# Performance work log

Measured on AMD Instinct MI355X. Metric: run time of the kernel, lower is better.

The kernel has to match this reference:

```python
import jax, jax.numpy as jnp
import numpy as np

B, S, D = 2, 2048, 1024
N_HEADS = 16
HEAD_DIM = D // N_HEADS  # 64, even for RoPE
THETA = 10000.0


def rope_tables(seq, head_dim, dtype=jnp.float32):
    half = head_dim // 2
    freqs = 1.0 / (THETA ** (jnp.arange(half, dtype=jnp.float32) / half))
    angles = jnp.arange(seq, dtype=jnp.float32)[:, None] * freqs[None, :]  # [S, half]
    return jnp.cos(angles).astype(dtype), jnp.sin(angles).astype(dtype)


def apply_rope_interleaved(x, cos, sin):
    # x: [b, h, s, d]; even/odd interleaving
    x_even = x[..., 0::2]
    x_odd = x[..., 1::2]
    r_even = x_even * cos - x_odd * sin
    r_odd = x_even * sin + x_odd * cos
    # interleave back: stack on last axis then reshape
    out = jnp.stack([r_even, r_odd], axis=-1).reshape(x.shape)
    return out


def setup_inputs() -> dict:
    key = jax.random.key(0)
    ks = jax.random.split(key, 6)
    scale = 1.0 / np.sqrt(D)
    return {
        "x": jax.random.normal(ks[0], (B, S, D), dtype=jnp.float32),
        "Wq": jax.random.normal(ks[1], (D, D), dtype=jnp.float32) * scale,
        "Wk": jax.random.normal(ks[2], (D, D), dtype=jnp.float32) * scale,
        "Wv": jax.random.normal(ks[3], (D, D), dtype=jnp.float32) * scale,
        "Wo": jax.random.normal(ks[4], (D, D), dtype=jnp.float32) * scale,
        "bo": jnp.zeros((D,), dtype=jnp.float32),
    }


def reference(x, Wq, Wk, Wv, Wo, bo):
    b, s, _ = x.shape
    # QKV projections (no bias), split heads -> [b, h, s, hd]
    def proj(W):
        return jnp.einsum('bsd,de->bse', x, W).reshape(b, s, N_HEADS, HEAD_DIM).transpose(0, 2, 1, 3)
    q, k, v = proj(Wq), proj(Wk), proj(Wv)

    cos, sin = rope_tables(s, HEAD_DIM, x.dtype)  # [s, hd//2]
    q = apply_rope_interleaved(q, cos, sin)
    k = apply_rope_interleaved(k, cos, sin)

    scale = 1.0 / jnp.sqrt(jnp.asarray(HEAD_DIM, dtype=x.dtype))
    scores = jnp.einsum('bhqd,bhkd->bhqk', q, k) * scale  # [b, h, s, s]
    causal = jnp.tril(jnp.ones((s, s), dtype=bool))
    scores = jnp.where(causal[None, None], scores, jnp.asarray(-jnp.inf, dtype=scores.dtype))
    attn = jax.nn.softmax(scores, axis=-1)
    ctx = jnp.einsum('bhqk,bhkd->bhqd', attn, v)  # [b, h, s, hd]
    ctx = ctx.transpose(0, 2, 1, 3).reshape(b, s, N_HEADS * HEAD_DIM)
    return jnp.einsum('bsd,de->bse', ctx, Wo) + bo
```

## Files before the change

### kernel.cpp

```cpp
#include <hip/hip_runtime.h>
#include <hip/hip_bf16.h>
#include <math.h>

constexpr int Bb   = 2;
constexpr int S    = 2048;
constexpr int D    = 1024;
constexpr int H    = 16;
constexpr int Dh   = 64;
constexpr int HALF = 32;
constexpr int M    = Bb * S;
constexpr int K    = 1024;
constexpr int N    = 1024;

typedef __attribute__((ext_vector_type(8))) short short8;
typedef __attribute__((ext_vector_type(4))) float f32x4;

__device__ __forceinline__ unsigned short f2bf(float f) {
    unsigned int u = __float_as_uint(f);
    unsigned int r = (u + 0x7fffu + ((u >> 16) & 1u)) >> 16;
    return (unsigned short)r;
}

__device__ __forceinline__ void gl_lds16(const unsigned short* g, unsigned short* lds_base) {
    __builtin_amdgcn_global_load_lds(
        (const __attribute__((address_space(1))) unsigned int*)g,
        (__attribute__((address_space(3))) unsigned int*)lds_base, 16, 0, 0);
}

__global__ __launch_bounds__(256) void prep_kernel(
    const float* __restrict__ x,
    const float* W0, const float* W1, const float* W2, const float* W3,
    unsigned short* __restrict__ xb,
    unsigned short* T0, unsigned short* T1, unsigned short* T2, unsigned short* T3,
    float* __restrict__ cosT, float* __restrict__ sinT)
{
    __shared__ float tile[64][65];
    const int bid = blockIdx.x;
    const int tid = threadIdx.x;

    if (bid < 256) {
        int idx = bid * 256 + tid;
        int s = idx >> 5;
        int i = idx & 31;
        double freq = exp(-(double)i * (log(10000.0) / 32.0));
        double ang  = (double)s * freq;
        cosT[idx] = (float)cos(ang);
        sinT[idx] = (float)sin(ang);
    } else if (bid < 256 + 4096) {
        size_t i = (size_t)(bid - 256) * 256 + tid;
        float4 v = *(const float4*)(x + i * 4);
        ushort4 pk;
        pk.x = f2bf(v.x); pk.y = f2bf(v.y); pk.z = f2bf(v.z); pk.w = f2bf(v.w);
        *(ushort4*)(xb + i * 4) = pk;
    } else {
        int wb = bid - 4352;
        int z  = wb >> 8;
        int rem = wb & 255;
        const float* W = (z == 0) ? W0 : (z == 1) ? W1 : (z == 2) ? W2 : W3;
        unsigned short* T = (z == 0) ? T0 : (z == 1) ? T1 : (z == 2) ? T2 : T3;
        const int bk = (rem >> 4) * 64;
        const int bn = (rem & 15) * 64;
        const int lr = tid >> 4;
        const int lc = (tid & 15) * 4;

        #pragma unroll
        for (int i = 0; i < 4; ++i) {
            int r = lr + i * 16;
            float4 v = *(const float4*)(W + (size_t)(bk + r) * N + bn + lc);
            tile[r][lc + 0] = v.x; tile[r][lc + 1] = v.y;
            tile[r][lc + 2] = v.z; tile[r][lc + 3] = v.w;
        }
        __syncthreads();
        #pragma unroll
        for (int i = 0; i < 4; ++i) {
            int nr = lr + i * 16;
            ushort4 pk;
            pk.x = f2bf(tile[lc + 0][nr]);
            pk.y = f2bf(tile[lc + 1][nr]);
            pk.z = f2bf(tile[lc + 2][nr]);
            pk.w = f2bf(tile[lc + 3][nr]);
            *(ushort4*)(T + (size_t)(bn + nr) * K + bk + lc) = pk;
        }
    }
}

__global__ __launch_bounds__(512, 2) void gemm_qkv_kernel(
    const unsigned short* __restrict__ A,
    const unsigned short* __restrict__ BT,
    unsigned short* outQ, unsigned short* outK, unsigned short* outV,
    const float* __restrict__ cosT, const float* __restrict__ sinT)
{
    constexpr int NT    = 16;
    constexpr int ASLOT = 256 * 64;
    constexpr int BSLOT = 192 * 64;
    __shared__ __align__(16) unsigned short As[2 * ASLOT];
    __shared__ __align__(16) unsigned short Bs[2 * BSLOT];

    const int tid  = threadIdx.x;
    const int wid  = tid >> 6;
    const int lane = tid & 63;
    const int col  = lane & 15;
    const int quad = lane >> 4;
    const int wr   = wid >> 2;
    const int wc   = wid & 3;

    const int mbase = blockIdx.y * 256;
    const int nbase = blockIdx.x * 192;

    const int srow8 = lane >> 3;
    const int sch8  = lane & 7;
    const unsigned short *pA[4], *pB[3];
    unsigned short *dA[4], *dB[3];
    #pragma unroll
    for (int w = 0; w < 4; ++w) {
        int r = wid * 32 + w * 8 + srow8;
        pA[w] = A + (size_t)(mbase + r) * K + ((sch8 + (r >> 1)) & 7) * 8;
        dA[w] = &As[(wid * 32 + w * 8) * 64];
    }
    #pragma unroll
    for (int w = 0; w < 3; ++w) {
        int r = wid * 24 + w * 8 + srow8;
        pB[w] = BT + (size_t)(nbase + r) * K + ((sch8 + (r >> 1)) & 7) * 8;
        dB[w] = &Bs[(wid * 24 + w * 8) * 64];
    }

    int aoff[2][8], boff[2][3];
    #pragma unroll
    for (int kh = 0; kh < 2; ++kh) {
        #pragma unroll
        for (int f = 0; f < 8; ++f) {
            int r = wr * 128 + f * 16 + col;
            aoff[kh][f] = r * 64 + (((kh * 4 + quad) - (r >> 1)) & 7) * 8;
        }
        #pragma unroll
        for (int n = 0; n < 3; ++n) {
            int r = wc * 48 + n * 16 + col;
            boff[kh][n] = r * 64 + (((kh * 4 + quad) - (r >> 1)) & 7) * 8;
        }
    }

    f32x4 acc[8][3];
    #pragma unroll
    for (int f = 0; f < 8; ++f)
        #pragma unroll
        for (int n = 0; n < 3; ++n) acc[f][n] = (f32x4)0.f;

    auto stageA = [&](int slot) {
        #pragma unroll
        for (int w = 0; w < 4; ++w) { gl_lds16(pA[w], dA[w] + slot * ASLOT); pA[w] += 64; }
    };
    auto stageB = [&](int slot) {
        #pragma unroll
        for (int w = 0; w < 3; ++w) { gl_lds16(pB[w], dB[w] + slot * BSLOT); pB[w] += 64; }
    };

    stageA(0); stageB(0);
    asm volatile("s_waitcnt vmcnt(0)" ::: "memory");
    __builtin_amdgcn_s_barrier();
    __builtin_amdgcn_sched_barrier(0);

    #pragma unroll 1
    for (int t = 0; t < NT; ++t) {
        const unsigned short* Ab = &As[(t & 1) * ASLOT];
        const unsigned short* Bc = &Bs[(t & 1) * BSLOT];
        const int ns = (t + 1) & 1;
        short8 af[4], bf[3];

        #pragma unroll
        for (int i = 0; i < 4; ++i) af[i] = *(const short8*)&Ab[aoff[0][i]];
        #pragma unroll
        for (int n = 0; n < 3; ++n) bf[n] = *(const short8*)&Bc[boff[0][n]];
        if (t < NT - 1) stageA(ns);
        __builtin_amdgcn_sched_barrier(0);
        __builtin_amdgcn_s_barrier();
        asm volatile("s_waitcnt lgkmcnt(0)" ::: "memory");
        __builtin_amdgcn_s_setprio(1);
        #pragma unroll
        for (int i = 0; i < 4; ++i)
            #pragma unroll
            for (int n = 0; n < 3; ++n)
                acc[i][n] = __builtin_amdgcn_mfma_f32_16x16x32_bf16(af[i], bf[n], acc[i][n], 0, 0, 0);
        __builtin_amdgcn_s_setprio(0);
        __builtin_amdgcn_sched_barrier(0);
        __builtin_amdgcn_s_barrier();
        __builtin_amdgcn_sched_barrier(0);

        #pragma unroll
        for (int i = 0; i < 4; ++i) af[i] = *(const short8*)&Ab[aoff[0][4 + i]];
        if (t < NT - 1) stageB(ns);
        __builtin_amdgcn_sched_barrier(0);
        __builtin_amdgcn_s_barrier();
        asm volatile("s_waitcnt lgkmcnt(0)" ::: "memory");
        __builtin_amdgcn_s_setprio(1);
        #pragma unroll
        for (int i = 0; i < 4; ++i)
            #pragma unroll
            for (int n = 0; n < 3; ++n)
                acc[4 + i][n] = __builtin_amdgcn_mfma_f32_16x16x32_bf16(af[i], bf[n], acc[4 + i][n], 0, 0, 0);
        __builtin_amdgcn_s_setprio(0);
        __builtin_amdgcn_sched_barrier(0);
        __builtin_amdgcn_s_barrier();
        __builtin_amdgcn_sched_barrier(0);

        #pragma unroll
        for (int i = 0; i < 4; ++i) af[i] = *(const short8*)&Ab[aoff[1][i]];
        #pragma unroll
        for (int n = 0; n < 3; ++n) bf[n] = *(const short8*)&Bc[boff[1][n]];
        __builtin_amdgcn_sched_barrier(0);
        __builtin_amdgcn_s_barrier();
        asm volatile("s_waitcnt lgkmcnt(0)" ::: "memory");
        __builtin_amdgcn_s_setprio(1);
        #pragma unroll
        for (int i = 0; i < 4; ++i)
            #pragma unroll
            for (int n = 0; n < 3; ++n)
                acc[i][n] = __builtin_amdgcn_mfma_f32_16x16x32_bf16(af[i], bf[n], acc[i][n], 0, 0, 0);
        __builtin_amdgcn_s_setprio(0);
        __builtin_amdgcn_sched_barrier(0);
        __builtin_amdgcn_s_barrier();
        __builtin_amdgcn_sched_barrier(0);

        #pragma unroll
        for (int i = 0; i < 4; ++i) af[i] = *(const short8*)&Ab[aoff[1][4 + i]];
        __builtin_amdgcn_sched_barrier(0);
        __builtin_amdgcn_s_barrier();
        asm volatile("s_waitcnt lgkmcnt(0)" ::: "memory");
        __builtin_amdgcn_s_setprio(1);
        #pragma unroll
        for (int i = 0; i < 4; ++i)
            #pragma unroll
            for (int n = 0; n < 3; ++n)
                acc[4 + i][n] = __builtin_amdgcn_mfma_f32_16x16x32_bf16(af[i], bf[n], acc[4 + i][n], 0, 0, 0);
        __builtin_amdgcn_s_setprio(0);
        if (t < NT - 1) { asm volatile("s_waitcnt vmcnt(0)" ::: "memory"); }
        __builtin_amdgcn_sched_barrier(0);
        __builtin_amdgcn_s_barrier();
        __builtin_amdgcn_sched_barrier(0);
    }

    #pragma unroll
    for (int n = 0; n < 3; ++n) {
        int n_g = nbase + wc * 48 + n * 16 + col;
        int z   = n_g >> 10;
        int nl  = n_g & 1023;
        int h = nl >> 6, dh0 = nl & 63;
        if (z < 2) {
            unsigned short* o = z ? outK : outQ;
            int p = dh0 >> 1;
            bool even = !(dh0 & 1);
            #pragma unroll
            for (int f = 0; f < 8; ++f)
                #pragma unroll
                for (int reg = 0; reg < 4; ++reg) {
                    int m_g = mbase + wr * 128 + f * 16 + quad * 4 + reg;
                    int b = m_g >> 11, s = m_g & 2047;
                    float v = acc[f][n][reg];
                    float part = __shfl_xor(v, 1, 64);
                    float c = cosT[s * HALF + p], sn = sinT[s * HALF + p];
                    float r = even ? (v * c - part * sn) : (v * c + part * sn);
                    o[((size_t)(b * H + h) * S + s) * Dh + dh0] = f2bf(r);
                }
        } else {
            #pragma unroll
            for (int f = 0; f < 8; ++f) {
                int m0 = mbase + wr * 128 + f * 16 + quad * 4;
                int b = m0 >> 11, s = m0 & 2047;
                ushort4 pk;
                pk.x = f2bf(acc[f][n][0]);
                pk.y = f2bf(acc[f][n][1]);
                pk.z = f2bf(acc[f][n][2]);
                pk.w = f2bf(acc[f][n][3]);
                *(ushort4*)&outV[((size_t)(b * H + h) * Dh + dh0) * S + s] = pk;
            }
        }
    }
}

__global__ __launch_bounds__(256) void gemm_out_kernel(
    const unsigned short* __restrict__ A,
    const unsigned short* __restrict__ BT,
    float* __restrict__ outO, const float* __restrict__ bias)
{
    constexpr int BK   = 64;
    constexpr int ABUF = 64 * BK;
    constexpr int BBUF = 64 * BK;
    __shared__ __align__(16) unsigned short As[2 * ABUF];
    __shared__ __align__(16) unsigned short Bs[2 * BBUF];

    const int tid  = threadIdx.x;
    const int wave = tid >> 6;
    const int lane = tid & 63;
    const int col  = lane & 15;
    const int quad = lane >> 4;
    const int wy   = wave >> 1;
    const int wx   = wave & 1;

    const int mbase = blockIdx.y * 64;
    const int nbase = blockIdx.x * 64;

    const int srow8 = lane >> 3;
    const int sch8  = lane & 7;

    const unsigned short *pA[2], *pB[2];
    unsigned short *dA[2], *dB[2];
    #pragma unroll
    for (int w = 0; w < 2; ++w) {
        int base = wave * 16 + w * 8;
        int tr = base + srow8;
        pA[w] = A  + (size_t)(mbase + tr) * K + ((sch8 + (tr >> 1)) & 7) * 8;
        pB[w] = BT + (size_t)(nbase + tr) * K + ((sch8 + (tr >> 1)) & 7) * 8;
        dA[w] = &As[base * BK];
        dB[w] = &Bs[base * BK];
    }

    int aoff[2][2], boff[2][2];
    #pragma unroll
    for (int ks = 0; ks < 2; ++ks) {
        #pragma unroll
        for (int mi = 0; mi < 2; ++mi) {
            int r = wy * 32 + mi * 16 + col;
            aoff[ks][mi] = r * BK + (((ks * 4 + quad) - (r >> 1)) & 7) * 8;
        }
        #pragma unroll
        for (int ni = 0; ni < 2; ++ni) {
            int r = wx * 32 + ni * 16 + col;
            boff[ks][ni] = r * BK + (((ks * 4 + quad) - (r >> 1)) & 7) * 8;
        }
    }

    f32x4 acc[2][2];
    #pragma unroll
    for (int mi = 0; mi < 2; ++mi)
        #pragma unroll
        for (int ni = 0; ni < 2; ++ni) acc[mi][ni] = (f32x4)0.f;

    auto stage = [&](int buf) {
        #pragma unroll
        for (int w = 0; w < 2; ++w) { gl_lds16(pA[w], dA[w] + buf * ABUF); pA[w] += BK; }
        #pragma unroll
        for (int w = 0; w < 2; ++w) { gl_lds16(pB[w], dB[w] + buf * BBUF); pB[w] += BK; }
    };
    auto compute = [&](int buf) {
        const unsigned short* Ac = &As[buf * ABUF];
        const unsigned short* Bc = &Bs[buf * BBUF];
        #pragma unroll
        for (int ks = 0; ks < 2; ++ks) {
            short8 af[2], bfr[2];
            #pragma unroll
            for (int mi = 0; mi < 2; ++mi) af[mi] = *(const short8*)&Ac[aoff[ks][mi]];
            #pragma unroll
            for (int ni = 0; ni < 2; ++ni) bfr[ni] = *(const short8*)&Bc[boff[ks][ni]];
            #pragma unroll
            for (int mi = 0; mi < 2; ++mi)
                #pragma unroll
                for (int ni = 0; ni < 2; ++ni)
                    acc[mi][ni] = __builtin_amdgcn_mfma_f32_16x16x32_bf16(af[mi], bfr[ni], acc[mi][ni], 0, 0, 0);
        }
    };

    stage(0);
    #pragma unroll 1
    for (int kk = 0; kk < 16; kk += 2) {
        __syncthreads();
        if (kk + 1 < 16) stage(1);
        compute(0);
        __syncthreads();
        if (kk + 2 < 16) stage(0);
        compute(1);
    }

    #pragma unroll
    for (int ni = 0; ni < 2; ++ni) {
        int n_g = nbase + wx * 32 + ni * 16 + col;
        float bv = bias[n_g];
        #pragma unroll
        for (int mi = 0; mi < 2; ++mi)
            #pragma unroll
            for (int reg = 0; reg < 4; ++reg) {
                int m_g = mbase + wy * 32 + mi * 16 + quad * 4 + reg;
                outO[(size_t)m_g * N + n_g] = acc[mi][ni][reg] + bv;
            }
    }
}

__global__ __launch_bounds__(512, 4) void attn_mfma_kernel(
    const unsigned short* __restrict__ q, const unsigned short* __restrict__ k,
    const unsigned short* __restrict__ vt,
    float* __restrict__ Opart, float* __restrict__ lpart)
{
    constexpr int TSZ = 64 * 64;
    __shared__ __align__(16) unsigned short Ks[2 * TSZ];
    __shared__ __align__(16) unsigned short Vs[2 * TSZ];
    __shared__ __align__(16) unsigned short Ps[8][16 * 64];

    const int tid  = threadIdx.x;
    const int wave = tid >> 6;
    const int lane = tid & 63;
    const int col  = lane & 15;
    const int quad = lane >> 4;
    const int r8   = lane >> 3, cp = lane & 7;

    const int pairh = blockIdx.x;
    const int pair  = pairh >> 1;
    const int hpar  = pairh & 1;
    const int bh = blockIdx.y;
    const unsigned short* qb = q  + (size_t)bh * S * Dh;
    const unsigned short* kb = k  + (size_t)bh * S * Dh;
    const unsigned short* vb = vt + (size_t)bh * Dh * S;

    unsigned short* dk = &Ks[(wave * 8) * 64];
    unsigned short* dv = &Vs[(wave * 8) * 64];

    int foff[2][4];
    #pragma unroll
    for (int ks = 0; ks < 2; ++ks)
        #pragma unroll
        for (int nt = 0; nt < 4; ++nt) {
            int r = nt * 16 + col;
            foff[ks][nt] = r * 64 + (((ks * 4 + quad) - r) & 7) * 8;
        }
    int poffW[4][4];
    #pragma unroll
    for (int nt = 0; nt < 4; ++nt)
        #pragma unroll
        for (int reg = 0; reg < 4; ++reg) {
            int row = quad * 4 + reg;
            poffW[nt][reg] = row * 64 + (((nt * 2 + (col >> 3)) ^ (row & 7)) << 3) + (col & 7);
        }
    int poffR[2];
    #pragma unroll
    for (int ks = 0; ks < 2; ++ks)
        poffR[ks] = col * 64 + (((ks * 4 + quad) ^ (col & 7)) << 3);

    for (int phase = 0; phase < 2; ++phase) {
        const int qt  = phase ? (15 - pair) : pair;
        const int wr0 = qt * 128 + wave * 16;
        const int NV  = qt + 1;

        const unsigned short *pk, *pv;
        {
            int r = wave * 8 + r8;
            pk = kb + (size_t)(hpar * 64 + r) * Dh + ((cp + r) & 7) * 8;
            pv = vb + (size_t)r * S + hpar * 64 + ((cp + r) & 7) * 8;
        }
        auto stageKV = [&](int buf) {
            gl_lds16(pk, dk + buf * TSZ);
            gl_lds16(pv, dv + buf * TSZ);
            pk += 128 * Dh;
            pv += 128;
        };

        __syncthreads();
        stageKV(0);

        short8 qfrag[2];
        #pragma unroll
        for (int ks = 0; ks < 2; ++ks)
            qfrag[ks] = *(const short8*)(qb + (size_t)(wr0 + col) * Dh + ks * 32 + quad * 8);

        f32x4 O[4];
        float lacc[4];
        #pragma unroll
        for (int nt = 0; nt < 4; ++nt) O[nt] = (f32x4)0.f;
        #pragma unroll
        for (int r = 0; r < 4; ++r) lacc[r] = 0.f;

        auto subtile = [&](const unsigned short* Kc, const unsigned short* Vc, int t) {
            f32x4 sacc[4];
            #pragma unroll
            for (int nt = 0; nt < 4; ++nt) sacc[nt] = (f32x4)0.f;
            #pragma unroll
            for (int ks = 0; ks < 2; ++ks)
                #pragma unroll
                for (int nt = 0; nt < 4; ++nt) {
                    short8 kf = *(const short8*)&Kc[foff[ks][nt]];
                    sacc[nt] = __builtin_amdgcn_mfma_f32_16x16x32_bf16(qfrag[ks], kf, sacc[nt], 0, 0, 0);
                }
            const bool edge = (t * 64 + 63 > wr0);
            float pb[4][4];
            #pragma unroll
            for (int nt = 0; nt < 4; ++nt) {
                int key_g = t * 64 + nt * 16 + col;
                #pragma unroll
                for (int reg = 0; reg < 4; ++reg) {
                    float e = __builtin_amdgcn_exp2f(
                        fmaf(sacc[nt][reg], 0.18033688011112042f, -11.541560327111707f));
                    if (edge && key_g > wr0 + quad * 4 + reg) e = 0.f;
                    pb[nt][reg] = e;
                }
            }
            #pragma unroll
            for (int reg = 0; reg < 4; ++reg)
                lacc[reg] += (pb[0][reg] + pb[1][reg]) + (pb[2][reg] + pb[3][reg]);
            #pragma unroll
            for (int nt = 0; nt < 4; ++nt)
                #pragma unroll
                for (int reg = 0; reg < 4; ++reg)
                    Ps[wave][poffW[nt][reg]] = f2bf(pb[nt][reg]);
            #pragma unroll
            for (int ks = 0; ks < 2; ++ks) {
                short8 pf = *(const short8*)&Ps[wave][poffR[ks]];
                #pragma unroll
                for (int nt = 0; nt < 4; ++nt) {
                    short8 vf = *(const short8*)&Vc[foff[ks][nt]];
                    O[nt] = __builtin_amdgcn_mfma_f32_16x16x32_bf16(pf, vf, O[nt], 0, 0, 0);
                }
            }
        };

        for (int j = 0; j < NV; ++j) {
            __syncthreads();
            if (j + 1 < NV) stageKV((j + 1) & 1);
            const int t = hpar + 2 * j;
            if (t * 64 <= wr0 + 15)
                subtile(&Ks[(j & 1) * TSZ], &Vs[(j & 1) * TSZ], t);
        }

        #pragma unroll
        for (int reg = 0; reg < 4; ++reg) {
            float s = lacc[reg];
            #pragma unroll
            for (int off = 1; off <= 8; off <<= 1)
                s += __shfl_xor(s, off, 64);
            lacc[reg] = s;
        }

        const size_t pb_base = (size_t)(hpar * 32 + bh) * S;
        #pragma unroll
        for (int reg = 0; reg < 4; ++reg) {
            int rg = wr0 + quad * 4 + reg;
            float* op = Opart + (pb_base + rg) * 64 + col;
            #pragma unroll
            for (int nt = 0; nt < 4; ++nt)
                op[nt * 16] = O[nt][reg];
            if (col == 0)
                lpart[pb_base + rg] = lacc[reg];
        }
    }
}

__global__ __launch_bounds__(256) void combine_kernel(
    const float* __restrict__ Opart, const float* __restrict__ lpart,
    unsigned short* __restrict__ ctx)
{
    int gid = blockIdx.x * 256 + threadIdx.x;
    int bh  = gid >> 15;
    int rem = gid & 32767;
    int qr  = rem >> 4;
    int dg  = (rem & 15) << 2;

    size_t i0 = ((size_t)bh * S + qr) * 64 + dg;
    size_t i1 = ((size_t)(32 + bh) * S + qr) * 64 + dg;
    float4 a = *(const float4*)(Opart + i0);
    float4 c = *(const float4*)(Opart + i1);
    float inv = 1.0f / (lpart[(size_t)bh * S + qr] + lpart[(size_t)(32 + bh) * S + qr]);

    int b = bh >> 4, hh = bh & 15;
    ushort4 pk;
    pk.x = f2bf((a.x + c.x) * inv);
    pk.y = f2bf((a.y + c.y) * inv);
    pk.z = f2bf((a.z + c.z) * inv);
    pk.w = f2bf((a.w + c.w) * inv);
    *(ushort4*)(ctx + ((size_t)b * S + qr) * 1024 + hh * 64 + dg) = pk;
}

extern "C" void kernel_launch(void* const* d_in, const int* in_sizes, int n_in,
                              void* d_out, int out_size, void* d_ws, size_t ws_size,
                              hipStream_t stream) {
    const float* x  = (const float*)d_in[0];
    const float* Wq = (const float*)d_in[1];
    const float* Wk = (const float*)d_in[2];
    const float* Wv = (const float*)d_in[3];
    const float* Wo = (const float*)d_in[4];
    const float* bo = (const float*)d_in[5];
    float* out = (float*)d_out;

    const size_t MK  = (size_t)M * K;
    const size_t NK  = (size_t)N * K;
    const size_t QKV = (size_t)Bb * H * S * Dh;

    unsigned short* xb   = (unsigned short*)d_ws;
    unsigned short* WqT  = xb  + MK;
    unsigned short* WkT  = WqT + NK;
    unsigned short* WvT  = WkT + NK;
    unsigned short* WoT  = WvT + NK;
    unsigned short* qbuf = WoT + NK;
    unsigned short* kbuf = qbuf + QKV;
    unsigned short* vtb  = kbuf + QKV;
    unsigned short* ctxb = vtb  + QKV;
    float* cosT  = (float*)(ctxb + QKV);
    float* sinT  = cosT + (size_t)S * HALF;
    float* Opart = sinT + (size_t)S * HALF;
    float* lpart = Opart + (size_t)2 * 32 * S * 64;

    prep_kernel<<<5376, 256, 0, stream>>>(x, Wq, Wk, Wv, Wo,
                                          xb, WqT, WkT, WvT, WoT, cosT, sinT);

    gemm_qkv_kernel<<<dim3(16, 16), 512, 0, stream>>>(
        xb, WqT, qbuf, kbuf, vtb, cosT, sinT);

    attn_mfma_kernel<<<dim3(16, Bb * H), 512, 0, stream>>>(qbuf, kbuf, vtb, Opart, lpart);

    combine_kernel<<<4096, 256, 0, stream>>>(Opart, lpart, ctxb);

    gemm_out_kernel<<<dim3(16, 64), 256, 0, stream>>>(ctxb, WoT, out, bo);
}
```

Measured before the change: 189.9 us.

## Split attention KV range three ways and store partial outputs in bf16

```diff
diff --git a/kernel.cpp b/kernel.cpp
--- a/kernel.cpp
+++ b/kernel.cpp
@@ -19,6 +19,9 @@
     unsigned int u = __float_as_uint(f);
     unsigned int r = (u + 0x7fffu + ((u >> 16) & 1u)) >> 16;
     return (unsigned short)r;
+}
+__device__ __forceinline__ float b2f(unsigned short u) {
+    return __uint_as_float((unsigned int)u << 16);
 }
 
 __device__ __forceinline__ void gl_lds16(const unsigned short* g, unsigned short* lds_base) {
@@ -383,10 +386,10 @@
     }
 }
 
-__global__ __launch_bounds__(512, 4) void attn_mfma_kernel(
+__global__ __launch_bounds__(512, 6) void attn_mfma_kernel(
     const unsigned short* __restrict__ q, const unsigned short* __restrict__ k,
     const unsigned short* __restrict__ vt,
-    float* __restrict__ Opart, float* __restrict__ lpart)
+    unsigned short* __restrict__ Opart, float* __restrict__ lpart)
 {
     constexpr int TSZ = 64 * 64;
     __shared__ __align__(16) unsigned short Ks[2 * TSZ];
@@ -400,9 +403,9 @@
     const int quad = lane >> 4;
     const int r8   = lane >> 3, cp = lane & 7;
 
-    const int pairh = blockIdx.x;
-    const int pair  = pairh >> 1;
-    const int hpar  = pairh & 1;
+    const int bx   = blockIdx.x;
+    const int pair = bx / 3;
+    const int hpar = bx % 3;
     const int bh = blockIdx.y;
     const unsigned short* qb = q  + (size_t)bh * S * Dh;
     const unsigned short* kb = k  + (size_t)bh * S * Dh;
@@ -435,7 +438,8 @@
     for (int phase = 0; phase < 2; ++phase) {
         const int qt  = phase ? (15 - pair) : pair;
         const int wr0 = qt * 128 + wave * 16;
-        const int NV  = qt + 1;
+        const int last = 2 * qt + 1;
+        const int NV  = (hpar <= last) ? ((last - hpar) / 3 + 1) : 0;
 
         const unsigned short *pk, *pv;
         {
@@ -446,12 +450,12 @@
         auto stageKV = [&](int buf) {
             gl_lds16(pk, dk + buf * TSZ);
             gl_lds16(pv, dv + buf * TSZ);
-            pk += 128 * Dh;
-            pv += 128;
+            pk += 192 * Dh;
+            pv += 192;
         };
 
         __syncthreads();
-        stageKV(0);
+        if (NV > 0) stageKV(0);
 
         short8 qfrag[2];
         #pragma unroll
@@ -511,7 +515,7 @@
         for (int j = 0; j < NV; ++j) {
             __syncthreads();
             if (j + 1 < NV) stageKV((j + 1) & 1);
-            const int t = hpar + 2 * j;
+            const int t = hpar + 3 * j;
             if (t * 64 <= wr0 + 15)
                 subtile(&Ks[(j & 1) * TSZ], &Vs[(j & 1) * TSZ], t);
         }
@@ -529,10 +533,10 @@
         #pragma unroll
         for (int reg = 0; reg < 4; ++reg) {
             int rg = wr0 + quad * 4 + reg;
-            float* op = Opart + (pb_base + rg) * 64 + col;
+            unsigned short* op = Opart + (pb_base + rg) * 64 + col;
             #pragma unroll
             for (int nt = 0; nt < 4; ++nt)
-                op[nt * 16] = O[nt][reg];
+                op[nt * 16] = f2bf(O[nt][reg]);
             if (col == 0)
                 lpart[pb_base + rg] = lacc[reg];
         }
@@ -540,7 +544,7 @@
 }
 
 __global__ __launch_bounds__(256) void combine_kernel(
-    const float* __restrict__ Opart, const float* __restrict__ lpart,
+    const unsigned short* __restrict__ Opart, const float* __restrict__ lpart,
     unsigned short* __restrict__ ctx)
 {
     int gid = blockIdx.x * 256 + threadIdx.x;
@@ -549,18 +553,22 @@
     int qr  = rem >> 4;
     int dg  = (rem & 15) << 2;
 
-    size_t i0 = ((size_t)bh * S + qr) * 64 + dg;
-    size_t i1 = ((size_t)(32 + bh) * S + qr) * 64 + dg;
-    float4 a = *(const float4*)(Opart + i0);
-    float4 c = *(const float4*)(Opart + i1);
-    float inv = 1.0f / (lpart[(size_t)bh * S + qr] + lpart[(size_t)(32 + bh) * S + qr]);
+    float sx = 0.f, sy = 0.f, sz = 0.f, sw = 0.f, lsum = 0.f;
+    #pragma unroll
+    for (int p = 0; p < 3; ++p) {
+        size_t rowb = (size_t)(p * 32 + bh) * S + qr;
+        ushort4 a = *(const ushort4*)(Opart + rowb * 64 + dg);
+        sx += b2f(a.x); sy += b2f(a.y); sz += b2f(a.z); sw += b2f(a.w);
+        lsum += lpart[rowb];
+    }
+    float inv = 1.0f / lsum;
 
     int b = bh >> 4, hh = bh & 15;
     ushort4 pk;
-    pk.x = f2bf((a.x + c.x) * inv);
-    pk.y = f2bf((a.y + c.y) * inv);
-    pk.z = f2bf((a.z + c.z) * inv);
-    pk.w = f2bf((a.w + c.w) * inv);
+    pk.x = f2bf(sx * inv);
+    pk.y = f2bf(sy * inv);
+    pk.z = f2bf(sz * inv);
+    pk.w = f2bf(sw * inv);
     *(ushort4*)(ctx + ((size_t)b * S + qr) * 1024 + hh * 64 + dg) = pk;
 }
 
@@ -588,10 +596,10 @@
     unsigned short* kbuf = qbuf + QKV;
     unsigned short* vtb  = kbuf + QKV;
     unsigned short* ctxb = vtb  + QKV;
-    float* cosT  = (float*)(ctxb + QKV);
-    float* sinT  = cosT + (size_t)S * HALF;
-    float* Opart = sinT + (size_t)S * HALF;
-    float* lpart = Opart + (size_t)2 * 32 * S * 64;
+    float* cosT = (float*)(ctxb + QKV);
+    float* sinT = cosT + (size_t)S * HALF;
+    unsigned short* Opart = (unsigned short*)(sinT + (size_t)S * HALF);
+    float* lpart = (float*)(Opart + (size_t)3 * 32 * S * 64);
 
     prep_kernel<<<5376, 256, 0, stream>>>(x, Wq, Wk, Wv, Wo,
                                           xb, WqT, WkT, WvT, WoT, cosT, sinT);
@@ -599,7 +607,7 @@
     gemm_qkv_kernel<<<dim3(16, 16), 512, 0, stream>>>(
         xb, WqT, qbuf, kbuf, vtb, cosT, sinT);
 
-    attn_mfma_kernel<<<dim3(16, Bb * H), 512, 0, stream>>>(qbuf, kbuf, vtb, Opart, lpart);
+    attn_mfma_kernel<<<dim3(24, Bb * H), 512, 0, stream>>>(qbuf, kbuf, vtb, Opart, lpart);
 
     combine_kernel<<<4096, 256, 0, stream>>>(Opart, lpart, ctxb);
 
```

Result: slower. 205.7 us (+8.4%).
